# Performance work log

Hardware: AMD Instinct MI355X
Metric: run time of the kernel (lower is better)

The kernel has to match this reference:

```python
import jax, jax.numpy as jnp
import numpy as np

K = 20000   # know_num
I = 50000   # item_num
D = 128     # emb_dim
N = K + I   # nodes in exer+know graphs (exercises first)
E1 = 320000 # edges in directed knowledge graph
E2 = 640000 # edges in each exer<->know graph


def setup_inputs() -> dict:
    key = jax.random.key(0)
    ks = jax.random.split(key, 20)
    s = 1.0 / np.sqrt(D)
    s2 = 1.0 / np.sqrt(2 * D)
    return {
        'kn_emb': jax.random.normal(ks[0], (K, D), jnp.float32),
        'exer_emb': jax.random.normal(ks[1], (I, D), jnp.float32),
        # GAT params: W is fc.weight.T ([in,out]); a is attn_fc.weight flattened ([2D])
        'W_dir': jax.random.normal(ks[2], (D, D), jnp.float32) * s,
        'a_dir': jax.random.normal(ks[3], (2 * D,), jnp.float32) * s2,
        'W_ke': jax.random.normal(ks[4], (D, D), jnp.float32) * s,
        'a_ke': jax.random.normal(ks[5], (2 * D,), jnp.float32) * s2,
        'W_ek': jax.random.normal(ks[6], (D, D), jnp.float32) * s,
        'a_ek': jax.random.normal(ks[7], (2 * D,), jnp.float32) * s2,
        # relation attention MLP: Linear(D,D)+bias, Tanh, Linear(D,1,no bias)
        'rel_W1': jax.random.normal(ks[8], (D, D), jnp.float32) * s,
        'rel_b1': jax.random.normal(ks[9], (D,), jnp.float32) * s,
        'rel_w2': jax.random.normal(ks[10], (D,), jnp.float32) * s,
        # edge lists (src, dst)
        'directed_src': jax.random.randint(ks[11], (E1,), 0, K),
        'directed_dst': jax.random.randint(ks[12], (E1,), 0, K),
        'ke_src': jax.random.randint(ks[13], (E2,), 0, N),
        'ke_dst': jax.random.randint(ks[14], (E2,), 0, N),
        'ek_src': jax.random.randint(ks[15], (E2,), 0, N),
        'ek_dst': jax.random.randint(ks[16], (E2,), 0, N),
    }


def _gat(h, W, a, src, dst, n):
    # GraphLayer: z = fc(h); e = leaky_relu(attn_fc([z_src; z_dst]));
    # alpha = softmax_e over dst; h_out = sum alpha * z_src
    z = h @ W                                   # [n_in, D]
    # split attn vector: cat([z_src,z_dst]) @ a == z_src@a[:D] + z_dst@a[D:]
    s_src = z @ a[:D]                           # [n_in]
    s_dst = z @ a[D:]                           # [n_in]
    e = jax.nn.leaky_relu(s_src[src] + s_dst[dst], 0.01)  # [E]
    m = jax.ops.segment_max(e, dst, num_segments=n)
    ex = jnp.exp(e - m[dst])
    den = jax.ops.segment_sum(ex, dst, num_segments=n)
    alpha = ex / den[dst]                       # segment softmax over in-edges
    return jax.ops.segment_sum(alpha[:, None] * z[src], dst, num_segments=n)


def reference(kn_emb, exer_emb, W_dir, a_dir, W_ke, a_ke, W_ek, a_ek,
              rel_W1, rel_b1, rel_w2,
              directed_src, directed_dst, ke_src, ke_dst, ek_src, ek_dst):
    A = _gat(kn_emb, W_dir, a_dir, directed_src, directed_dst, K)      # [K,D]
    ek = jnp.concatenate([exer_emb, kn_emb], axis=0)                   # [N,D]
    B = _gat(ek, W_ke, a_ke, ke_src, ke_dst, N)[I:]                    # [K,D]
    Cfull = _gat(ek, W_ek, a_ek, ek_src, ek_dst, N)                    # [N,D]
    s1 = jnp.tanh(A @ rel_W1 + rel_b1) @ rel_w2                        # [K]
    s2 = jnp.tanh(B @ rel_W1 + rel_b1) @ rel_w2                        # [K]
    score = jax.nn.softmax(jnp.stack([s1, s2], axis=1), axis=1)        # [K,2]
    kn_out = score[:, 0:1] * A + score[:, 1:2] * B                     # [K,D]
    exer_out = Cfull[:I]                                               # [I,D]
    return (kn_out, exer_out)
```

## Files before the change

kernel.cpp:

```cpp
#include <hip/hip_runtime.h>
#include <math.h>

#define KN   20000
#define IN_  50000
#define DD   128
#define NN   70000
#define E1N  320000
#define E2N  640000

#define GB0  313
#define GB1  1094
#define GB2  1094

typedef _Float16 f16x8 __attribute__((ext_vector_type(8)));
typedef float floatx4 __attribute__((ext_vector_type(4)));

__device__ __forceinline__ unsigned f2bf(float x) {
  unsigned u = __float_as_uint(x);
  return (u + 0x7FFFu + ((u >> 16) & 1u)) >> 16;
}
__device__ __forceinline__ unsigned packbf(float a, float b) {
  return f2bf(a) | (f2bf(b) << 16);
}
__device__ __forceinline__ float bf_lo(unsigned u) { return __uint_as_float(u << 16); }
__device__ __forceinline__ float bf_hi(unsigned u) { return __uint_as_float(u & 0xFFFF0000u); }

__global__ __launch_bounds__(256) void prep(
    const float* __restrict__ W0, const float* __restrict__ W1,
    const float* __restrict__ W2, const float* __restrict__ W3,
    short* __restrict__ wfr,
    const int* __restrict__ ddst, const int* __restrict__ kedst, const int* __restrict__ ekdst,
    int* __restrict__ cnt_dir, int* __restrict__ cnt_ke, int* __restrict__ cnt_ek,
    unsigned short* __restrict__ rank_dir, unsigned short* __restrict__ rank_ke,
    unsigned short* __restrict__ rank_ek)
{
  int b = blockIdx.x;
  if (b < 32) {
    int wsel = b >> 3;
    const float* W = (wsel == 0) ? W0 : (wsel == 1) ? W1 : (wsel == 2) ? W2 : W3;
    int fi = (b & 7) * 256 + threadIdx.x;
    int l = fi & 63, chunk = (fi >> 6) & 3, t = fi >> 8;
    int col = t * 16 + (l & 15);
    int kbase = chunk * 32 + (l >> 4) * 8;
    f16x8 hv;
#pragma unroll
    for (int j = 0; j < 8; ++j) hv[j] = (_Float16)W[(kbase + j) * 128 + col];
    ((f16x8*)(wfr + wsel * 16384))[fi] = hv;
    return;
  }
  int i = (b - 32) * 256 + threadIdx.x;
  if (i < E1N) {
    rank_dir[i] = (unsigned short)atomicAdd(&cnt_dir[ddst[i]], 1);
  } else if (i < E1N + E2N) {
    int e = i - E1N;
    int d = kedst[e];
    if (d >= IN_) rank_ke[e] = (unsigned short)atomicAdd(&cnt_ke[d - IN_], 1);
  } else {
    int e = i - E1N - E2N;
    int d = ekdst[e];
    if (d < IN_) rank_ek[e] = (unsigned short)atomicAdd(&cnt_ek[d], 1);
  }
}

__global__ __launch_bounds__(256, 4) void gemm3(
    const float* __restrict__ kn, const float* __restrict__ ex,
    const short* __restrict__ wfr,
    const float* __restrict__ a_dir, const float* __restrict__ a_ke, const float* __restrict__ a_ek,
    unsigned* __restrict__ zb_dir, unsigned* __restrict__ zb_ke, unsigned* __restrict__ zb_ek,
    float* __restrict__ sds, float* __restrict__ sdd,
    float* __restrict__ sks, float* __restrict__ skd,
    float* __restrict__ ses, float* __restrict__ sed)
{
  __shared__ short sW[16384];
  const int bid = blockIdx.x;
  const int tid = threadIdx.x;

  const float *h1, *h2, *avec;
  unsigned* zb;
  float *ssrc, *sdst;
  const short* wf;
  int split, rows, tile;
  if (bid < GB0) {
    tile = bid; rows = KN; split = KN; h1 = kn; h2 = kn;
    wf = wfr; avec = a_dir; zb = zb_dir; ssrc = sds; sdst = sdd;
  } else if (bid < GB0 + GB1) {
    tile = bid - GB0; rows = NN; split = IN_; h1 = ex; h2 = kn;
    wf = wfr + 16384; avec = a_ke; zb = zb_ke; ssrc = sks; sdst = skd;
  } else {
    tile = bid - GB0 - GB1; rows = NN; split = IN_; h1 = ex; h2 = kn;
    wf = wfr + 32768; avec = a_ek; zb = zb_ek; ssrc = ses; sdst = sed;
  }

  {
    const int4* gs = (const int4*)wf;
    int4* ls = (int4*)sW;
#pragma unroll
    for (int it = 0; it < 8; ++it) ls[it * 256 + tid] = gs[it * 256 + tid];
  }
  __syncthreads();

  const int lane = tid & 63;
  const int wv = tid >> 6;
  const int q = lane >> 4;
  const int m = lane & 15;
  const int r = tile * 64 + wv * 16 + m;
  const int rc = (r < rows) ? r : (rows - 1);
  const float* hp = (rc < split) ? (h1 + (size_t)rc * 128)
                                 : (h2 + (size_t)(rc - split) * 128);

  floatx4 acc[8];
#pragma unroll
  for (int t = 0; t < 8; ++t) { acc[t][0]=0.f; acc[t][1]=0.f; acc[t][2]=0.f; acc[t][3]=0.f; }

#pragma unroll
  for (int chunk = 0; chunk < 4; ++chunk) {
    float4 v0 = *(const float4*)(hp + chunk * 32 + q * 8);
    float4 v1 = *(const float4*)(hp + chunk * 32 + q * 8 + 4);
    float vs[8] = {v0.x, v0.y, v0.z, v0.w, v1.x, v1.y, v1.z, v1.w};
    f16x8 ahi, alo;
#pragma unroll
    for (int j = 0; j < 8; ++j) {
      _Float16 h = (_Float16)vs[j];
      ahi[j] = h;
      alo[j] = (_Float16)(vs[j] - (float)h);
    }
#pragma unroll
    for (int t = 0; t < 8; ++t) {
      f16x8 bh = ((const f16x8*)sW)[(t * 4 + chunk) * 64 + lane];
      acc[t] = __builtin_amdgcn_mfma_f32_16x16x32_f16(bh, ahi, acc[t], 0, 0, 0);
      acc[t] = __builtin_amdgcn_mfma_f32_16x16x32_f16(bh, alo, acc[t], 0, 0, 0);
    }
  }

  if (r < rows) {
    unsigned* zrow = zb + (size_t)r * 64;
#pragma unroll
    for (int t = 0; t < 8; ++t) {
      uint2 pk;
      pk.x = packbf(acc[t][0], acc[t][1]);
      pk.y = packbf(acc[t][2], acc[t][3]);
      *(uint2*)(zrow + t * 8 + q * 2) = pk;
    }
  }
  float d1 = 0.f, d2 = 0.f;
#pragma unroll
  for (int t = 0; t < 8; ++t) {
    float4 wa = *(const float4*)(avec + t * 16 + q * 4);
    float4 wb = *(const float4*)(avec + 128 + t * 16 + q * 4);
    d1 += acc[t][0] * wa.x + acc[t][1] * wa.y + acc[t][2] * wa.z + acc[t][3] * wa.w;
    d2 += acc[t][0] * wb.x + acc[t][1] * wb.y + acc[t][2] * wb.z + acc[t][3] * wb.w;
  }
  d1 += __shfl_xor(d1, 16, 64); d1 += __shfl_xor(d1, 32, 64);
  d2 += __shfl_xor(d2, 16, 64); d2 += __shfl_xor(d2, 32, 64);
  if (q == 0 && r < rows) { ssrc[r] = d1; sdst[r] = d2; }
}

__global__ __launch_bounds__(256) void alloc_off(
    const int* __restrict__ cnt_dir, int2* __restrict__ sc_dir,
    const int* __restrict__ cnt_ke,  int2* __restrict__ sc_ke,
    const int* __restrict__ cnt_ek,  int2* __restrict__ sc_ek,
    int* __restrict__ totals)
{
  int b = blockIdx.x;
  const int* cnt; int2* sc; int* tot; int n, i0;
  if (b < 79)       { cnt = cnt_dir; sc = sc_dir; tot = totals + 0; n = KN;  i0 = b * 256; }
  else if (b < 158) { cnt = cnt_ke;  sc = sc_ke;  tot = totals + 1; n = KN;  i0 = (b - 79) * 256; }
  else              { cnt = cnt_ek;  sc = sc_ek;  tot = totals + 2; n = IN_; i0 = (b - 158) * 256; }
  int i = i0 + threadIdx.x;
  int lane = threadIdx.x & 63;
  int v = (i < n) ? cnt[i] : 0;
  int x = v;
#pragma unroll
  for (int o = 1; o < 64; o <<= 1) {
    int t = __shfl_up(x, o, 64);
    if (lane >= o) x += t;
  }
  int base = 0;
  if (lane == 63) base = atomicAdd(tot, x);
  base = __shfl(base, 63, 64);
  if (i < n) sc[i] = make_int2(base + x - v, v);
}

__global__ __launch_bounds__(256) void fill_edges(
    const int* __restrict__ dsrc, const int* __restrict__ ddst,
    const int* __restrict__ kesrc, const int* __restrict__ kedst,
    const int* __restrict__ eksrc, const int* __restrict__ ekdst,
    const unsigned short* __restrict__ rank_dir, const unsigned short* __restrict__ rank_ke,
    const unsigned short* __restrict__ rank_ek,
    const float* __restrict__ sds, const float* __restrict__ sdd,
    const float* __restrict__ sks, const float* __restrict__ skd,
    const float* __restrict__ ses, const float* __restrict__ sed,
    const int2* __restrict__ sc_dir, int2* __restrict__ ep_dir,
    const int2* __restrict__ sc_ke,  int2* __restrict__ ep_ke,
    const int2* __restrict__ sc_ek,  int2* __restrict__ ep_ek)
{
  int i = blockIdx.x * 256 + threadIdx.x;
  if (i < E1N) {
    int d = ddst[i];
    int s = dsrc[i];
    float x = sds[s] + sdd[d];
    ep_dir[sc_dir[d].x + rank_dir[i]] = make_int2(s, __float_as_int(x));
  } else if (i < E1N + E2N) {
    int e = i - E1N;
    int d = kedst[e];
    if (d >= IN_) {
      int s = kesrc[e];
      float x = sks[s] + skd[d];
      ep_ke[sc_ke[d - IN_].x + rank_ke[e]] = make_int2(s, __float_as_int(x));
    }
  } else {
    int e = i - E1N - E2N;
    int d = ekdst[e];
    if (d < IN_) {
      int s = eksrc[e];
      float x = ses[s] + sed[d];
      ep_ek[sc_ek[d].x + rank_ek[e]] = make_int2(s, __float_as_int(x));
    }
  }
}

__global__ __launch_bounds__(256) void gat_gather(
    const int2* __restrict__ sc_dir, const int2* __restrict__ ep_dir,
    const unsigned* __restrict__ zb_dir, float* __restrict__ A,
    const int2* __restrict__ sc_ke, const int2* __restrict__ ep_ke,
    const unsigned* __restrict__ zb_ke, float* __restrict__ Bm,
    const int2* __restrict__ sc_ek, const int2* __restrict__ ep_ek,
    const unsigned* __restrict__ zb_ek, float* __restrict__ Cout)
{
  int gw = (blockIdx.x * 256 + threadIdx.x) >> 6;
  int lane = threadIdx.x & 63;
  int h = lane >> 5;
  int ln31 = lane & 31;
  int gh = (lane >> 4) & 1;
  int gl = lane & 15;

  const int2 *scp, *ep;
  const unsigned* zb;
  float* out;
  int s0;
  if (gw < 10000)      { s0 = 2 * gw;             scp = sc_dir; ep = ep_dir; zb = zb_dir; out = A; }
  else if (gw < 20000) { s0 = 2 * (gw - 10000);   scp = sc_ke;  ep = ep_ke;  zb = zb_ke;  out = Bm; }
  else                 { s0 = 2 * (gw - 20000);   scp = sc_ek;  ep = ep_ek;  zb = zb_ek;  out = Cout; }

  int4 scc = *(const int4*)((const int*)scp + 2 * s0);
  int b   = h ? scc.z : scc.x;
  int cnt = h ? scc.w : scc.y;
  int lim = (cnt < 32) ? cnt : 32;

  int   src_l = 0;
  float w_l   = 0.f;
  if (ln31 < lim) {
    int2 pe = ep[b + ln31];
    src_l = pe.x;
    float x = __int_as_float(pe.y);
    x = (x > 0.f) ? x : 0.01f * x;
    w_l = __expf(x);
  }

  float den = w_l;
  den += __shfl_xor(den, 1, 64);
  den += __shfl_xor(den, 2, 64);
  den += __shfl_xor(den, 4, 64);
  den += __shfl_xor(den, 8, 64);
  den += __shfl_xor(den, 16, 64);

  float av[8];
#pragma unroll
  for (int k = 0; k < 8; ++k) av[k] = 0.f;

  for (int j0 = 0; j0 < lim; j0 += 8) {
    int base = h * 32 + j0 + gh * 4;
    int   s1 = __shfl(src_l, base + 0, 64); float w1 = __shfl(w_l, base + 0, 64);
    int   s2 = __shfl(src_l, base + 1, 64); float w2 = __shfl(w_l, base + 1, 64);
    int   s3 = __shfl(src_l, base + 2, 64); float w3 = __shfl(w_l, base + 2, 64);
    int   s4 = __shfl(src_l, base + 3, 64); float w4 = __shfl(w_l, base + 3, 64);
    uint4 za = *(const uint4*)(zb + (size_t)s1 * 64 + gl * 4);
    uint4 zc = *(const uint4*)(zb + (size_t)s2 * 64 + gl * 4);
    uint4 ze = *(const uint4*)(zb + (size_t)s3 * 64 + gl * 4);
    uint4 zg = *(const uint4*)(zb + (size_t)s4 * 64 + gl * 4);
    av[0] += w1 * bf_lo(za.x); av[1] += w1 * bf_hi(za.x);
    av[2] += w1 * bf_lo(za.y); av[3] += w1 * bf_hi(za.y);
    av[4] += w1 * bf_lo(za.z); av[5] += w1 * bf_hi(za.z);
    av[6] += w1 * bf_lo(za.w); av[7] += w1 * bf_hi(za.w);
    av[0] += w2 * bf_lo(zc.x); av[1] += w2 * bf_hi(zc.x);
    av[2] += w2 * bf_lo(zc.y); av[3] += w2 * bf_hi(zc.y);
    av[4] += w2 * bf_lo(zc.z); av[5] += w2 * bf_hi(zc.z);
    av[6] += w2 * bf_lo(zc.w); av[7] += w2 * bf_hi(zc.w);
    av[0] += w3 * bf_lo(ze.x); av[1] += w3 * bf_hi(ze.x);
    av[2] += w3 * bf_lo(ze.y); av[3] += w3 * bf_hi(ze.y);
    av[4] += w3 * bf_lo(ze.z); av[5] += w3 * bf_hi(ze.z);
    av[6] += w3 * bf_lo(ze.w); av[7] += w3 * bf_hi(ze.w);
    av[0] += w4 * bf_lo(zg.x); av[1] += w4 * bf_hi(zg.x);
    av[2] += w4 * bf_lo(zg.y); av[3] += w4 * bf_hi(zg.y);
    av[4] += w4 * bf_lo(zg.z); av[5] += w4 * bf_hi(zg.z);
    av[6] += w4 * bf_lo(zg.w); av[7] += w4 * bf_hi(zg.w);
  }

  if (cnt > 32) {
    float dtail = 0.f;
    int e = b + cnt;
    for (int i = b + 32 + gh; i < e; i += 2) {
      int2 p1 = ep[i];
      float x1 = __int_as_float(p1.y);
      x1 = (x1 > 0.f) ? x1 : 0.01f * x1;
      float w1 = __expf(x1);
      uint4 za = *(const uint4*)(zb + (size_t)p1.x * 64 + gl * 4);
      dtail += w1;
      av[0] += w1 * bf_lo(za.x); av[1] += w1 * bf_hi(za.x);
      av[2] += w1 * bf_lo(za.y); av[3] += w1 * bf_hi(za.y);
      av[4] += w1 * bf_lo(za.z); av[5] += w1 * bf_hi(za.z);
      av[6] += w1 * bf_lo(za.w); av[7] += w1 * bf_hi(za.w);
    }
    den += dtail + __shfl_xor(dtail, 16, 64);
  }

#pragma unroll
  for (int k = 0; k < 8; ++k) av[k] += __shfl_xor(av[k], 16, 64);

  if (cnt > 0) {
    float inv = 1.f / den;
#pragma unroll
    for (int k = 0; k < 8; ++k) av[k] *= inv;
  }

  if (gh == 0) {
    int seg = s0 + h;
    float* op = out + (size_t)seg * 128 + gl * 8;
    *(float4*)op       = make_float4(av[0], av[1], av[2], av[3]);
    *(float4*)(op + 4) = make_float4(av[4], av[5], av[6], av[7]);
  }
}

__global__ __launch_bounds__(256, 2) void relgemm_combine(
    const float* __restrict__ Am, const float* __restrict__ Bm,
    const short* __restrict__ wfr_rel,
    const float* __restrict__ rb1, const float* __restrict__ rw2,
    float* __restrict__ out)
{
  __shared__ short sW[16384];
  const int tid = threadIdx.x;
  {
    const int4* gs = (const int4*)wfr_rel;
    int4* ls = (int4*)sW;
#pragma unroll
    for (int it = 0; it < 8; ++it) ls[it * 256 + tid] = gs[it * 256 + tid];
  }
  __syncthreads();

  const int lane = tid & 63;
  const int wv = tid >> 6;
  const int q = lane >> 4;
  const int m = lane & 15;
  const int r = blockIdx.x * 64 + wv * 16 + m;
  const int rc = (r < KN) ? r : (KN - 1);
  const float* hA = Am + (size_t)rc * 128;
  const float* hB = Bm + (size_t)rc * 128;

  floatx4 accA[8], accB[8];
#pragma unroll
  for (int t = 0; t < 8; ++t) {
    accA[t][0]=0.f; accA[t][1]=0.f; accA[t][2]=0.f; accA[t][3]=0.f;
    accB[t][0]=0.f; accB[t][1]=0.f; accB[t][2]=0.f; accB[t][3]=0.f;
  }

#pragma unroll
  for (int chunk = 0; chunk < 4; ++chunk) {
    float4 a0 = *(const float4*)(hA + chunk * 32 + q * 8);
    float4 a1 = *(const float4*)(hA + chunk * 32 + q * 8 + 4);
    float4 b0 = *(const float4*)(hB + chunk * 32 + q * 8);
    float4 b1 = *(const float4*)(hB + chunk * 32 + q * 8 + 4);
    float as[8] = {a0.x, a0.y, a0.z, a0.w, a1.x, a1.y, a1.z, a1.w};
    float bs[8] = {b0.x, b0.y, b0.z, b0.w, b1.x, b1.y, b1.z, b1.w};
    f16x8 ahiA, aloA, ahiB, aloB;
#pragma unroll
    for (int j = 0; j < 8; ++j) {
      _Float16 ha = (_Float16)as[j];
      ahiA[j] = ha; aloA[j] = (_Float16)(as[j] - (float)ha);
      _Float16 hb = (_Float16)bs[j];
      ahiB[j] = hb; aloB[j] = (_Float16)(bs[j] - (float)hb);
    }
#pragma unroll
    for (int t = 0; t < 8; ++t) {
      f16x8 bh = ((const f16x8*)sW)[(t * 4 + chunk) * 64 + lane];
      accA[t] = __builtin_amdgcn_mfma_f32_16x16x32_f16(bh, ahiA, accA[t], 0, 0, 0);
      accA[t] = __builtin_amdgcn_mfma_f32_16x16x32_f16(bh, aloA, accA[t], 0, 0, 0);
      accB[t] = __builtin_amdgcn_mfma_f32_16x16x32_f16(bh, ahiB, accB[t], 0, 0, 0);
      accB[t] = __builtin_amdgcn_mfma_f32_16x16x32_f16(bh, aloB, accB[t], 0, 0, 0);
    }
  }

  float p1 = 0.f, p2 = 0.f;
#pragma unroll
  for (int t = 0; t < 8; ++t) {
    float4 bb = *(const float4*)(rb1 + t * 16 + q * 4);
    float4 ww = *(const float4*)(rw2 + t * 16 + q * 4);
    p1 += tanhf(accA[t][0] + bb.x) * ww.x + tanhf(accA[t][1] + bb.y) * ww.y +
          tanhf(accA[t][2] + bb.z) * ww.z + tanhf(accA[t][3] + bb.w) * ww.w;
    p2 += tanhf(accB[t][0] + bb.x) * ww.x + tanhf(accB[t][1] + bb.y) * ww.y +
          tanhf(accB[t][2] + bb.z) * ww.z + tanhf(accB[t][3] + bb.w) * ww.w;
  }
  p1 += __shfl_xor(p1, 16, 64); p1 += __shfl_xor(p1, 32, 64);
  p2 += __shfl_xor(p2, 16, 64); p2 += __shfl_xor(p2, 32, 64);

  float mx = fmaxf(p1, p2);
  float e1 = __expf(p1 - mx), e2 = __expf(p2 - mx);
  float al = e1 / (e1 + e2), be = e2 / (e1 + e2);

  if (r < KN) {
#pragma unroll
    for (int t = 0; t < 8; ++t) {
      int col = t * 16 + q * 4;
      float4 avv = *(const float4*)(Am + (size_t)r * 128 + col);
      float4 bvv = *(const float4*)(Bm + (size_t)r * 128 + col);
      *(float4*)(out + (size_t)r * 128 + col) =
          make_float4(al * avv.x + be * bvv.x, al * avv.y + be * bvv.y,
                      al * avv.z + be * bvv.z, al * avv.w + be * bvv.w);
    }
  }
}

extern "C" void kernel_launch(void* const* d_in, const int* in_sizes, int n_in,
                              void* d_out, int out_size, void* d_ws, size_t ws_size,
                              hipStream_t stream) {
  const float* kn    = (const float*)d_in[0];
  const float* ex    = (const float*)d_in[1];
  const float* W_dir = (const float*)d_in[2];
  const float* a_dir = (const float*)d_in[3];
  const float* W_ke  = (const float*)d_in[4];
  const float* a_ke  = (const float*)d_in[5];
  const float* W_ek  = (const float*)d_in[6];
  const float* a_ek  = (const float*)d_in[7];
  const float* rW1   = (const float*)d_in[8];
  const float* rb1   = (const float*)d_in[9];
  const float* rw2   = (const float*)d_in[10];
  const int* dsrc    = (const int*)d_in[11];
  const int* ddst    = (const int*)d_in[12];
  const int* kesrc   = (const int*)d_in[13];
  const int* kedst   = (const int*)d_in[14];
  const int* eksrc   = (const int*)d_in[15];
  const int* ekdst   = (const int*)d_in[16];
  float* out = (float*)d_out;

  char* p = (char*)d_ws;
  auto alloc = [&](size_t bytes) {
    char* r = p;
    p += (bytes + 255) & ~(size_t)255;
    return r;
  };
  unsigned* zb_dir = (unsigned*)alloc((size_t)KN * 64 * 4);
  unsigned* zb_ke  = (unsigned*)alloc((size_t)NN * 64 * 4);
  unsigned* zb_ek  = (unsigned*)alloc((size_t)NN * 64 * 4);
  float* Am    = (float*)alloc((size_t)KN * 128 * 4);
  float* Bmat  = (float*)alloc((size_t)KN * 128 * 4);
  short* wfr   = (short*)alloc((size_t)4 * 16384 * 2);
  float* sds = (float*)alloc(KN * 4);
  float* sdd = (float*)alloc(KN * 4);
  float* sks = (float*)alloc(NN * 4);
  float* skd = (float*)alloc(NN * 4);
  float* ses = (float*)alloc(NN * 4);
  float* sed = (float*)alloc(NN * 4);
  int* cntblk  = (int*)alloc((size_t)(2 * KN + IN_ + 64) * 4);
  int* cnt_dir = cntblk;
  int* cnt_ke  = cntblk + KN;
  int* cnt_ek  = cntblk + 2 * KN;
  int* totals  = cntblk + 2 * KN + IN_;
  int2* sc_dir = (int2*)alloc((size_t)KN * 8);
  int2* sc_ke  = (int2*)alloc((size_t)KN * 8);
  int2* sc_ek  = (int2*)alloc((size_t)IN_ * 8);
  unsigned short* rank_dir = (unsigned short*)alloc((size_t)E1N * 2);
  unsigned short* rank_ke  = (unsigned short*)alloc((size_t)E2N * 2);
  unsigned short* rank_ek  = (unsigned short*)alloc((size_t)E2N * 2);
  int2* ep_dir = (int2*)alloc((size_t)E1N * 8);
  int2* ep_ke  = (int2*)alloc((size_t)E2N * 8);
  int2* ep_ek  = (int2*)alloc((size_t)E2N * 8);

  hipMemsetAsync(cntblk, 0, (size_t)(2 * KN + IN_ + 64) * 4, stream);

  prep<<<32 + (E1N + 2 * E2N) / 256, 256, 0, stream>>>(
      W_dir, W_ke, W_ek, rW1, wfr,
      ddst, kedst, ekdst, cnt_dir, cnt_ke, cnt_ek,
      rank_dir, rank_ke, rank_ek);

  gemm3<<<GB0 + GB1 + GB2, 256, 0, stream>>>(
      kn, ex, wfr, a_dir, a_ke, a_ek,
      zb_dir, zb_ke, zb_ek,
      sds, sdd, sks, skd, ses, sed);

  alloc_off<<<354, 256, 0, stream>>>(cnt_dir, sc_dir, cnt_ke, sc_ke, cnt_ek, sc_ek, totals);

  fill_edges<<<(E1N + 2 * E2N) / 256, 256, 0, stream>>>(
      dsrc, ddst, kesrc, kedst, eksrc, ekdst,
      rank_dir, rank_ke, rank_ek,
      sds, sdd, sks, skd, ses, sed,
      sc_dir, ep_dir, sc_ke, ep_ke, sc_ek, ep_ek);

  gat_gather<<<11250, 256, 0, stream>>>(
      sc_dir, ep_dir, zb_dir, Am,
      sc_ke,  ep_ke,  zb_ke,  Bmat,
      sc_ek,  ep_ek,  zb_ek,  out + (size_t)KN * 128);

  relgemm_combine<<<313, 256, 0, stream>>>(Am, Bmat, wfr + 3 * 16384, rb1, rw2, out);
}
```

Baseline: 275.4 us.

## Fuse edge counting into GEMM kernel and vectorize edge processing by four

The per-destination edge counting and rank assignment moves out of the prep kernel into the projection GEMM kernel. Blocks are interleaved so that in every group of 13, 8 do GEMM tiles and 5 do counting, letting the atomic-heavy counting overlap with MFMA work. Both the counting and fill_edges now handle four edges per thread using int4 and ushort4 loads and stores, which cuts thread count and index overhead. The cost is a more complex block mapping, some idle blocks, and LDS allocated for counting blocks that do not use it, which may lower occupancy.

```diff
diff --git a/kernel.cpp b/kernel.cpp
--- a/kernel.cpp
+++ b/kernel.cpp
@@ -11,6 +11,11 @@
 #define GB0  313
 #define GB1  1094
 #define GB2  1094
+#define GTILES 2501
+
+#define GROUPS 313
+#define MGRID  (GROUPS*13)
+#define CNT_CHUNKS 1563
 
 typedef _Float16 f16x8 __attribute__((ext_vector_type(8)));
 typedef float floatx4 __attribute__((ext_vector_type(4)));
@@ -28,52 +33,76 @@
 __global__ __launch_bounds__(256) void prep(
     const float* __restrict__ W0, const float* __restrict__ W1,
     const float* __restrict__ W2, const float* __restrict__ W3,
-    short* __restrict__ wfr,
-    const int* __restrict__ ddst, const int* __restrict__ kedst, const int* __restrict__ ekdst,
-    int* __restrict__ cnt_dir, int* __restrict__ cnt_ke, int* __restrict__ cnt_ek,
-    unsigned short* __restrict__ rank_dir, unsigned short* __restrict__ rank_ke,
-    unsigned short* __restrict__ rank_ek)
+    short* __restrict__ wfr)
 {
   int b = blockIdx.x;
-  if (b < 32) {
-    int wsel = b >> 3;
-    const float* W = (wsel == 0) ? W0 : (wsel == 1) ? W1 : (wsel == 2) ? W2 : W3;
-    int fi = (b & 7) * 256 + threadIdx.x;
-    int l = fi & 63, chunk = (fi >> 6) & 3, t = fi >> 8;
-    int col = t * 16 + (l & 15);
-    int kbase = chunk * 32 + (l >> 4) * 8;
-    f16x8 hv;
-#pragma unroll
-    for (int j = 0; j < 8; ++j) hv[j] = (_Float16)W[(kbase + j) * 128 + col];
-    ((f16x8*)(wfr + wsel * 16384))[fi] = hv;
-    return;
-  }
-  int i = (b - 32) * 256 + threadIdx.x;
-  if (i < E1N) {
-    rank_dir[i] = (unsigned short)atomicAdd(&cnt_dir[ddst[i]], 1);
-  } else if (i < E1N + E2N) {
-    int e = i - E1N;
-    int d = kedst[e];
-    if (d >= IN_) rank_ke[e] = (unsigned short)atomicAdd(&cnt_ke[d - IN_], 1);
-  } else {
-    int e = i - E1N - E2N;
-    int d = ekdst[e];
-    if (d < IN_) rank_ek[e] = (unsigned short)atomicAdd(&cnt_ek[d], 1);
-  }
-}
-
-__global__ __launch_bounds__(256, 4) void gemm3(
+  int wsel = b >> 3;
+  const float* W = (wsel == 0) ? W0 : (wsel == 1) ? W1 : (wsel == 2) ? W2 : W3;
+  int fi = (b & 7) * 256 + threadIdx.x;
+  int l = fi & 63, chunk = (fi >> 6) & 3, t = fi >> 8;
+  int col = t * 16 + (l & 15);
+  int kbase = chunk * 32 + (l >> 4) * 8;
+  f16x8 hv;
+#pragma unroll
+  for (int j = 0; j < 8; ++j) hv[j] = (_Float16)W[(kbase + j) * 128 + col];
+  ((f16x8*)(wfr + wsel * 16384))[fi] = hv;
+}
+
+__global__ __launch_bounds__(256, 4) void gemm3_count(
     const float* __restrict__ kn, const float* __restrict__ ex,
     const short* __restrict__ wfr,
     const float* __restrict__ a_dir, const float* __restrict__ a_ke, const float* __restrict__ a_ek,
     unsigned* __restrict__ zb_dir, unsigned* __restrict__ zb_ke, unsigned* __restrict__ zb_ek,
     float* __restrict__ sds, float* __restrict__ sdd,
     float* __restrict__ sks, float* __restrict__ skd,
-    float* __restrict__ ses, float* __restrict__ sed)
+    float* __restrict__ ses, float* __restrict__ sed,
+    const int* __restrict__ ddst, const int* __restrict__ kedst, const int* __restrict__ ekdst,
+    int* __restrict__ cnt_dir, int* __restrict__ cnt_ke, int* __restrict__ cnt_ek,
+    unsigned short* __restrict__ rank_dir, unsigned short* __restrict__ rank_ke,
+    unsigned short* __restrict__ rank_ek)
 {
   __shared__ short sW[16384];
-  const int bid = blockIdx.x;
+  const int g = blockIdx.x / 13;
+  const int r = blockIdx.x % 13;
   const int tid = threadIdx.x;
+
+  if (r >= 8) {
+    int cidx = g * 5 + (r - 8);
+    if (cidx >= CNT_CHUNKS) return;
+    int t = cidx * 256 + tid;
+    if (t < 80000) {
+      int e0 = t * 4;
+      int4 d4 = *(const int4*)(ddst + e0);
+      ushort4 rk;
+      rk.x = (unsigned short)atomicAdd(&cnt_dir[d4.x], 1);
+      rk.y = (unsigned short)atomicAdd(&cnt_dir[d4.y], 1);
+      rk.z = (unsigned short)atomicAdd(&cnt_dir[d4.z], 1);
+      rk.w = (unsigned short)atomicAdd(&cnt_dir[d4.w], 1);
+      *(ushort4*)(rank_dir + e0) = rk;
+    } else if (t < 240000) {
+      int e0 = (t - 80000) * 4;
+      int4 d4 = *(const int4*)(kedst + e0);
+      ushort4 rk = make_ushort4(0, 0, 0, 0);
+      if (d4.x >= IN_) rk.x = (unsigned short)atomicAdd(&cnt_ke[d4.x - IN_], 1);
+      if (d4.y >= IN_) rk.y = (unsigned short)atomicAdd(&cnt_ke[d4.y - IN_], 1);
+      if (d4.z >= IN_) rk.z = (unsigned short)atomicAdd(&cnt_ke[d4.z - IN_], 1);
+      if (d4.w >= IN_) rk.w = (unsigned short)atomicAdd(&cnt_ke[d4.w - IN_], 1);
+      *(ushort4*)(rank_ke + e0) = rk;
+    } else if (t < 400000) {
+      int e0 = (t - 240000) * 4;
+      int4 d4 = *(const int4*)(ekdst + e0);
+      ushort4 rk = make_ushort4(0, 0, 0, 0);
+      if (d4.x < IN_) rk.x = (unsigned short)atomicAdd(&cnt_ek[d4.x], 1);
+      if (d4.y < IN_) rk.y = (unsigned short)atomicAdd(&cnt_ek[d4.y], 1);
+      if (d4.z < IN_) rk.z = (unsigned short)atomicAdd(&cnt_ek[d4.z], 1);
+      if (d4.w < IN_) rk.w = (unsigned short)atomicAdd(&cnt_ek[d4.w], 1);
+      *(ushort4*)(rank_ek + e0) = rk;
+    }
+    return;
+  }
+
+  const int bid = g * 8 + r;
+  if (bid >= GTILES) return;
 
   const float *h1, *h2, *avec;
   unsigned* zb;
@@ -103,8 +132,8 @@
   const int wv = tid >> 6;
   const int q = lane >> 4;
   const int m = lane & 15;
-  const int r = tile * 64 + wv * 16 + m;
-  const int rc = (r < rows) ? r : (rows - 1);
+  const int rr = tile * 64 + wv * 16 + m;
+  const int rc = (rr < rows) ? rr : (rows - 1);
   const float* hp = (rc < split) ? (h1 + (size_t)rc * 128)
                                  : (h2 + (size_t)(rc - split) * 128);
 
@@ -132,8 +161,8 @@
     }
   }
 
-  if (r < rows) {
-    unsigned* zrow = zb + (size_t)r * 64;
+  if (rr < rows) {
+    unsigned* zrow = zb + (size_t)rr * 64;
 #pragma unroll
     for (int t = 0; t < 8; ++t) {
       uint2 pk;
@@ -152,7 +181,7 @@
   }
   d1 += __shfl_xor(d1, 16, 64); d1 += __shfl_xor(d1, 32, 64);
   d2 += __shfl_xor(d2, 16, 64); d2 += __shfl_xor(d2, 32, 64);
-  if (q == 0 && r < rows) { ssrc[r] = d1; sdst[r] = d2; }
+  if (q == 0 && rr < rows) { ssrc[rr] = d1; sdst[rr] = d2; }
 }
 
 __global__ __launch_bounds__(256) void alloc_off(
@@ -194,28 +223,34 @@
     const int2* __restrict__ sc_ke,  int2* __restrict__ ep_ke,
     const int2* __restrict__ sc_ek,  int2* __restrict__ ep_ek)
 {
-  int i = blockIdx.x * 256 + threadIdx.x;
-  if (i < E1N) {
-    int d = ddst[i];
-    int s = dsrc[i];
-    float x = sds[s] + sdd[d];
-    ep_dir[sc_dir[d].x + rank_dir[i]] = make_int2(s, __float_as_int(x));
-  } else if (i < E1N + E2N) {
-    int e = i - E1N;
-    int d = kedst[e];
-    if (d >= IN_) {
-      int s = kesrc[e];
-      float x = sks[s] + skd[d];
-      ep_ke[sc_ke[d - IN_].x + rank_ke[e]] = make_int2(s, __float_as_int(x));
-    }
-  } else {
-    int e = i - E1N - E2N;
-    int d = ekdst[e];
-    if (d < IN_) {
-      int s = eksrc[e];
-      float x = ses[s] + sed[d];
-      ep_ek[sc_ek[d].x + rank_ek[e]] = make_int2(s, __float_as_int(x));
-    }
+  int t = blockIdx.x * 256 + threadIdx.x;
+  if (t < 80000) {
+    int e0 = t * 4;
+    int4 s4 = *(const int4*)(dsrc + e0);
+    int4 d4 = *(const int4*)(ddst + e0);
+    ushort4 rk = *(const ushort4*)(rank_dir + e0);
+    ep_dir[sc_dir[d4.x].x + rk.x] = make_int2(s4.x, __float_as_int(sds[s4.x] + sdd[d4.x]));
+    ep_dir[sc_dir[d4.y].x + rk.y] = make_int2(s4.y, __float_as_int(sds[s4.y] + sdd[d4.y]));
+    ep_dir[sc_dir[d4.z].x + rk.z] = make_int2(s4.z, __float_as_int(sds[s4.z] + sdd[d4.z]));
+    ep_dir[sc_dir[d4.w].x + rk.w] = make_int2(s4.w, __float_as_int(sds[s4.w] + sdd[d4.w]));
+  } else if (t < 240000) {
+    int e0 = (t - 80000) * 4;
+    int4 s4 = *(const int4*)(kesrc + e0);
+    int4 d4 = *(const int4*)(kedst + e0);
+    ushort4 rk = *(const ushort4*)(rank_ke + e0);
+    if (d4.x >= IN_) ep_ke[sc_ke[d4.x - IN_].x + rk.x] = make_int2(s4.x, __float_as_int(sks[s4.x] + skd[d4.x]));
+    if (d4.y >= IN_) ep_ke[sc_ke[d4.y - IN_].x + rk.y] = make_int2(s4.y, __float_as_int(sks[s4.y] + skd[d4.y]));
+    if (d4.z >= IN_) ep_ke[sc_ke[d4.z - IN_].x + rk.z] = make_int2(s4.z, __float_as_int(sks[s4.z] + skd[d4.z]));
+    if (d4.w >= IN_) ep_ke[sc_ke[d4.w - IN_].x + rk.w] = make_int2(s4.w, __float_as_int(sks[s4.w] + skd[d4.w]));
+  } else if (t < 400000) {
+    int e0 = (t - 240000) * 4;
+    int4 s4 = *(const int4*)(eksrc + e0);
+    int4 d4 = *(const int4*)(ekdst + e0);
+    ushort4 rk = *(const ushort4*)(rank_ek + e0);
+    if (d4.x < IN_) ep_ek[sc_ek[d4.x].x + rk.x] = make_int2(s4.x, __float_as_int(ses[s4.x] + sed[d4.x]));
+    if (d4.y < IN_) ep_ek[sc_ek[d4.y].x + rk.y] = make_int2(s4.y, __float_as_int(ses[s4.y] + sed[d4.y]));
+    if (d4.z < IN_) ep_ek[sc_ek[d4.z].x + rk.z] = make_int2(s4.z, __float_as_int(ses[s4.z] + sed[d4.z]));
+    if (d4.w < IN_) ep_ek[sc_ek[d4.w].x + rk.w] = make_int2(s4.w, __float_as_int(ses[s4.w] + sed[d4.w]));
   }
 }
 
@@ -476,19 +511,18 @@
 
   hipMemsetAsync(cntblk, 0, (size_t)(2 * KN + IN_ + 64) * 4, stream);
 
-  prep<<<32 + (E1N + 2 * E2N) / 256, 256, 0, stream>>>(
-      W_dir, W_ke, W_ek, rW1, wfr,
+  prep<<<32, 256, 0, stream>>>(W_dir, W_ke, W_ek, rW1, wfr);
+
+  gemm3_count<<<MGRID, 256, 0, stream>>>(
+      kn, ex, wfr, a_dir, a_ke, a_ek,
+      zb_dir, zb_ke, zb_ek,
+      sds, sdd, sks, skd, ses, sed,
       ddst, kedst, ekdst, cnt_dir, cnt_ke, cnt_ek,
       rank_dir, rank_ke, rank_ek);
 
-  gemm3<<<GB0 + GB1 + GB2, 256, 0, stream>>>(
-      kn, ex, wfr, a_dir, a_ke, a_ek,
-      zb_dir, zb_ke, zb_ek,
-      sds, sdd, sks, skd, ses, sed);
-
   alloc_off<<<354, 256, 0, stream>>>(cnt_dir, sc_dir, cnt_ke, sc_ke, cnt_ek, sc_ek, totals);
 
-  fill_edges<<<(E1N + 2 * E2N) / 256, 256, 0, stream>>>(
+  fill_edges<<<1563, 256, 0, stream>>>(
       dsrc, ddst, kesrc, kedst, eksrc, ekdst,
       rank_dir, rank_ke, rank_ek,
       sds, sdd, sks, skd, ses, sed,
```

After: 262.3 us. 1.05x faster.
